# Kernel tuning notes

Measured on AMD Instinct MI355X. Metric: run time of the kernel, lower is better.

The kernel has to match this reference:

```python
import jax, jax.numpy as jnp
import numpy as np

B, NQ, NKV, D, H = 2, 2048, 2048, 2048, 16
HD = D // H


def setup_inputs() -> dict:
    key = jax.random.key(0)
    ks = jax.random.split(key, 9)
    return {
        "x": jax.random.normal(ks[0], (B, NQ, D), jnp.float32),
        "k": jax.random.normal(ks[1], (B, H, NKV, HD), jnp.float32),
        "v": jax.random.normal(ks[2], (B, H, NKV, HD), jnp.float32),
        "tier_labels": jax.random.randint(ks[3], (B, NKV), 0, 3),
        "padding_mask": jnp.zeros((B, NKV), dtype=bool),
        "q_w": jax.random.normal(ks[4], (D, D), jnp.float32) * (D ** -0.5),
        "q_b": jax.random.normal(ks[5], (D,), jnp.float32) * 0.02,
        "out_w": jax.random.normal(ks[6], (D, D), jnp.float32) * (D ** -0.5),
        "out_b": jax.random.normal(ks[7], (D,), jnp.float32) * 0.02,
        "tier_bias": jax.random.normal(ks[8], (3,), jnp.float32) * 0.1,
    }


def reference(x, k, v, tier_labels, padding_mask, q_w, q_b, out_w, out_b, tier_bias):
    b, n_q, d = x.shape
    h, n_kv, hd = k.shape[1], k.shape[2], k.shape[3]
    scale = hd ** -0.5
    # q projection: torch Linear is x @ W.T + b
    q = x @ q_w.T + q_b                         # [b, n_q, d]
    q = q.reshape(b, n_q, h, hd).transpose(0, 2, 1, 3)  # [b, h, n_q, hd]
    attn = jnp.einsum("bhqd,bhkd->bhqk", q, k) * scale  # [b, h, n_q, n_kv]
    # additive tier bias gathered per kv token
    attn = attn + tier_bias[tier_labels][:, None, None, :]
    # causal mask: triu(-inf, diagonal=n_kv - n_q + 1)
    causal = jnp.triu(jnp.full((n_q, n_kv), -jnp.inf, dtype=x.dtype), k=n_kv - n_q + 1)
    attn = attn + causal
    # padding mask -> -inf
    attn = jnp.where(padding_mask[:, None, None, :], -jnp.inf, attn)
    attn = jax.nn.softmax(attn, axis=-1)
    out = jnp.einsum("bhqk,bhkd->bhqd", attn, v)  # [b, h, n_q, hd]
    out = out.transpose(0, 2, 1, 3).reshape(b, n_q, d)
    return out @ out_w.T + out_b
```

## Files before the change

### kernel.cpp

```cpp
#include <hip/hip_runtime.h>
#include <stdint.h>

typedef unsigned short u16;
typedef __attribute__((ext_vector_type(8))) short short8;
typedef __attribute__((ext_vector_type(4))) float f32x4;

#define B_   2
#define NQ_  2048
#define NKV_ 2048
#define D_   2048
#define H_   16
#define HD_  128
#define MM_  (B_*NQ_)

__device__ __forceinline__ u16 f2bf(float f) {
  uint32_t u = __float_as_uint(f);
  u += 0x7fffu + ((u >> 16) & 1u);
  return (u16)(u >> 16);
}

__device__ __forceinline__ void gload_lds16(const void* g, void* l) {
  __builtin_amdgcn_global_load_lds(
      (const __attribute__((address_space(1))) void*)g,
      (__attribute__((address_space(3))) void*)l, 16, 0, 0);
}

__global__ __launch_bounds__(256) void cast_bf16(const float* __restrict__ src,
                                                 u16* __restrict__ dst, int n8) {
  int i = blockIdx.x * 256 + threadIdx.x;
  if (i >= n8) return;
  const float4* s = (const float4*)src + (size_t)i * 2;
  float4 a = s[0], b = s[1];
  short8 o;
  o[0] = (short)f2bf(a.x); o[1] = (short)f2bf(a.y);
  o[2] = (short)f2bf(a.z); o[3] = (short)f2bf(a.w);
  o[4] = (short)f2bf(b.x); o[5] = (short)f2bf(b.y);
  o[6] = (short)f2bf(b.z); o[7] = (short)f2bf(b.w);
  *((short8*)dst + i) = o;
}

__global__ __launch_bounds__(256) void build_bias(const int* __restrict__ labels,
                                                  const unsigned char* __restrict__ mask,
                                                  const float* __restrict__ tb,
                                                  float* __restrict__ out, int n) {
  int i = blockIdx.x * 256 + threadIdx.x;
  if (i < n) out[i] = mask[i] ? -1e30f : tb[labels[i]];
}

template<int OUT_BF16>
__global__ __launch_bounds__(256, 2) void gemm_bt(
    const u16* __restrict__ A, const u16* __restrict__ W,
    const float* __restrict__ bias, void* __restrict__ Cout,
    int M, int N, int K)
{
  __shared__ u16 As[128 * 64];
  __shared__ u16 Bs[128 * 64];
  const int tid = threadIdx.x;
  const int w = tid >> 6, l = tid & 63;
  const int lr = l & 15, lg = l >> 4;
  const int nbn = N >> 7;
  const int nwg = gridDim.x;
  int bid = blockIdx.x;
  int swz = (bid & 7) * (nwg >> 3) + (bid >> 3);
  const int bm = swz / nbn, bn = swz % nbn;
  const int wm = w >> 1, wn = w & 1;

  f32x4 acc[4][4] = {};

  const int sr = w * 32 + (l >> 3);
  const int sc = l & 7;

  for (int kt = 0; kt < K; kt += 64) {
#pragma unroll
    for (int i = 0; i < 4; ++i) {
      int r = sr + i * 8;
      int gc = kt + ((sc ^ (r & 7)) << 3);
      gload_lds16(A + (size_t)(bm * 128 + r) * K + gc, (char*)As + (w * 32 + i * 8) * 128);
      gload_lds16(W + (size_t)(bn * 128 + r) * K + gc, (char*)Bs + (w * 32 + i * 8) * 128);
    }
    __syncthreads();
#pragma unroll
    for (int ks = 0; ks < 2; ++ks) {
      short8 av[4], bv[4];
#pragma unroll
      for (int mf = 0; mf < 4; ++mf) {
        int row = wm * 64 + mf * 16 + lr;
        int pch = (ks * 4 + lg) ^ (row & 7);
        av[mf] = *(const short8*)((const char*)As + row * 128 + pch * 16);
      }
#pragma unroll
      for (int nf = 0; nf < 4; ++nf) {
        int row = wn * 64 + nf * 16 + lr;
        int pch = (ks * 4 + lg) ^ (row & 7);
        bv[nf] = *(const short8*)((const char*)Bs + row * 128 + pch * 16);
      }
#pragma unroll
      for (int mf = 0; mf < 4; ++mf)
#pragma unroll
        for (int nf = 0; nf < 4; ++nf)
          acc[mf][nf] = __builtin_amdgcn_mfma_f32_16x16x32_bf16(av[mf], bv[nf], acc[mf][nf], 0, 0, 0);
    }
    __syncthreads();
  }

  const int row0 = bm * 128 + wm * 64;
  const int col0 = bn * 128 + wn * 64;
#pragma unroll
  for (int nf = 0; nf < 4; ++nf) {
    int col = col0 + nf * 16 + lr;
    float bb = bias[col];
#pragma unroll
    for (int mf = 0; mf < 4; ++mf) {
#pragma unroll
      for (int r = 0; r < 4; ++r) {
        size_t row = (size_t)(row0 + mf * 16 + lg * 4 + r);
        float vv = acc[mf][nf][r] + bb;
        if (OUT_BF16) ((u16*)Cout)[row * N + col] = f2bf(vv);
        else          ((float*)Cout)[row * N + col] = vv;
      }
    }
  }
}

__global__ __launch_bounds__(256, 2) void attn_fwd(
    const u16* __restrict__ Q, const u16* __restrict__ Kg,
    const u16* __restrict__ Vg, const float* __restrict__ biaskv,
    u16* __restrict__ AO)
{
  __shared__ u16 Ks[64 * 128];
  __shared__ u16 Vt[128 * 72];
  __shared__ u16 Ps[4][16 * 72];

  const int tid = threadIdx.x;
  const int w = tid >> 6, l = tid & 63;
  const int lr = l & 15, lg = l >> 4;

  int bid = blockIdx.x;
  int swz = (bid & 7) * 128 + (bid >> 3);
  const int qt = 31 - (swz & 31);
  const int h  = (swz >> 5) & 15;
  const int b  = swz >> 9;

  const size_t kvbase = ((size_t)(b * H_ + h)) * NKV_ * HD_;
  const u16* Kh = Kg + kvbase;
  const u16* Vh = Vg + kvbase;
  const float* bkv = biaskv + b * NKV_;

  const int q0 = qt * 64 + w * 16;
  short8 aq[4];
  {
    const u16* qp = Q + (size_t)(b * NQ_ + q0 + lr) * D_ + h * HD_ + lg * 8;
#pragma unroll
    for (int ks = 0; ks < 4; ++ks) aq[ks] = *(const short8*)(qp + ks * 32);
  }

  f32x4 o[8] = {};
  float m[4], ln[4];
#pragma unroll
  for (int r = 0; r < 4; ++r) { m[r] = -1e30f; ln[r] = 0.f; }

  const int ntile = qt + 1;
  for (int kvt = 0; kvt < ntile; ++kvt) {
    const int kv0 = kvt * 64;
#pragma unroll
    for (int i = 0; i < 4; ++i) {
      int r = w * 16 + i * 4 + lg;
      int c = lr ^ (r & 7);
      gload_lds16(Kh + (size_t)(kv0 + r) * HD_ + c * 8, (char*)Ks + (w * 16 + i * 4) * 256);
    }
    {
      const u16* vp = Vh + (size_t)(kv0 + l) * HD_ + w * 32;
#pragma unroll
      for (int j = 0; j < 4; ++j) {
        short8 vv = *(const short8*)(vp + j * 8);
#pragma unroll
        for (int e = 0; e < 8; ++e)
          Vt[(w * 32 + j * 8 + e) * 72 + l] = (u16)vv[e];
      }
    }
    __syncthreads();

    f32x4 s[4];
#pragma unroll
    for (int nf = 0; nf < 4; ++nf) {
      f32x4 c = {};
#pragma unroll
      for (int ks = 0; ks < 4; ++ks) {
        int row = nf * 16 + lr;
        int pch = (ks * 4 + lg) ^ (row & 7);
        short8 bv = *(const short8*)((const char*)Ks + row * 256 + pch * 16);
        c = __builtin_amdgcn_mfma_f32_16x16x32_bf16(aq[ks], bv, c, 0, 0, 0);
      }
      s[nf] = c;
    }

    float sv[4][4];
#pragma unroll
    for (int nf = 0; nf < 4; ++nf) {
      int kv = kv0 + nf * 16 + lr;
      float bb = bkv[kv];
#pragma unroll
      for (int r = 0; r < 4; ++r) {
        float v = s[nf][r] * 0.08838834764831845f + bb;
        if (kvt == ntile - 1) {
          int q = q0 + lg * 4 + r;
          if (kv > q) v = -1e30f;
        }
        sv[nf][r] = v;
      }
    }

    float pm[4];
#pragma unroll
    for (int r = 0; r < 4; ++r)
      pm[r] = fmaxf(fmaxf(sv[0][r], sv[1][r]), fmaxf(sv[2][r], sv[3][r]));
#pragma unroll
    for (int off = 1; off < 16; off <<= 1)
#pragma unroll
      for (int r = 0; r < 4; ++r)
        pm[r] = fmaxf(pm[r], __shfl_xor(pm[r], off, 64));

    float alpha[4], mn[4], ps[4];
#pragma unroll
    for (int r = 0; r < 4; ++r) {
      mn[r] = fmaxf(m[r], pm[r]);
      alpha[r] = __expf(m[r] - mn[r]);
      m[r] = mn[r];
      ps[r] = 0.f;
    }

    u16* Pw = &Ps[w][0];
#pragma unroll
    for (int nf = 0; nf < 4; ++nf)
#pragma unroll
      for (int r = 0; r < 4; ++r) {
        float p = __expf(sv[nf][r] - mn[r]);
        ps[r] += p;
        Pw[(lg * 4 + r) * 72 + nf * 16 + lr] = f2bf(p);
      }

#pragma unroll
    for (int off = 1; off < 16; off <<= 1)
#pragma unroll
      for (int r = 0; r < 4; ++r)
        ps[r] += __shfl_xor(ps[r], off, 64);

#pragma unroll
    for (int r = 0; r < 4; ++r) ln[r] = ln[r] * alpha[r] + ps[r];

#pragma unroll
    for (int cf = 0; cf < 8; ++cf)
#pragma unroll
      for (int r = 0; r < 4; ++r)
        o[cf][r] *= alpha[r];

#pragma unroll
    for (int ks = 0; ks < 2; ++ks) {
      short8 ap = *(const short8*)((const char*)Pw + lr * 144 + ks * 64 + lg * 16);
#pragma unroll
      for (int nf = 0; nf < 8; ++nf) {
        short8 bv = *(const short8*)((const char*)Vt + (nf * 16 + lr) * 144 + ks * 64 + lg * 16);
        o[nf] = __builtin_amdgcn_mfma_f32_16x16x32_bf16(ap, bv, o[nf], 0, 0, 0);
      }
    }
    __syncthreads();
  }

#pragma unroll
  for (int r = 0; r < 4; ++r) {
    float inv = ln[r] > 0.f ? 1.f / ln[r] : 0.f;
    size_t row = (size_t)(b * NQ_ + q0 + lg * 4 + r);
#pragma unroll
    for (int nf = 0; nf < 8; ++nf)
      AO[row * D_ + h * HD_ + nf * 16 + lr] = f2bf(o[nf][r] * inv);
  }
}

extern "C" void kernel_launch(void* const* d_in, const int* in_sizes, int n_in,
                              void* d_out, int out_size, void* d_ws, size_t ws_size,
                              hipStream_t stream) {
  const float* x     = (const float*)d_in[0];
  const float* k     = (const float*)d_in[1];
  const float* v     = (const float*)d_in[2];
  const int*   labels = (const int*)d_in[3];
  const unsigned char* mask = (const unsigned char*)d_in[4];
  const float* q_w   = (const float*)d_in[5];
  const float* q_b   = (const float*)d_in[6];
  const float* out_w = (const float*)d_in[7];
  const float* out_b = (const float*)d_in[8];
  const float* tbias = (const float*)d_in[9];

  char* ws = (char*)d_ws;
  u16* x_bf  = (u16*)(ws + 0);
  u16* qw_bf = (u16*)(ws + 16777216);
  u16* ow_bf = (u16*)(ws + 25165824);
  u16* k_bf  = (u16*)(ws + 33554432);
  u16* v_bf  = (u16*)(ws + 50331648);
  u16* q_bf  = (u16*)(ws + 67108864);
  u16* ao_bf = (u16*)(ws + 83886080);
  float* bkv = (float*)(ws + 100663296);

  cast_bf16<<<4096, 256, 0, stream>>>(x,     x_bf,  1048576);
  cast_bf16<<<2048, 256, 0, stream>>>(q_w,   qw_bf,  524288);
  cast_bf16<<<2048, 256, 0, stream>>>(out_w, ow_bf,  524288);
  cast_bf16<<<4096, 256, 0, stream>>>(k,     k_bf,  1048576);
  cast_bf16<<<4096, 256, 0, stream>>>(v,     v_bf,  1048576);
  build_bias<<<16, 256, 0, stream>>>(labels, mask, tbias, bkv, B_ * NKV_);

  gemm_bt<1><<<512, 256, 0, stream>>>(x_bf, qw_bf, q_b, (void*)q_bf, MM_, D_, D_);
  attn_fwd<<<1024, 256, 0, stream>>>(q_bf, k_bf, v_bf, bkv, ao_bf);
  gemm_bt<0><<<512, 256, 0, stream>>>(ao_bf, ow_bf, out_b, d_out, MM_, D_, D_);
}
```

Before: 404.0 us.

## Pair causal q-tiles per block, double-buffer K/V, compute softmax in registers with exp2

Each attention block now handles two query tiles (qt and 31-qt) that share K/V loads, which balances causal work across blocks and halves the grid. The K/V tiles are double-buffered so global loads for the next tile overlap compute on the current one. The softmax scale and log2e are folded into the Q projection epilogue and the bias, so the kernel can use exp2. QK^T is computed transposed so P stays in registers and is permuted with lane shuffles instead of going through LDS. MFMA sections get raised wave priority via s_setprio. The cost is higher register pressure from two accumulator sets and extra shuffle traffic.

```diff
diff --git a/kernel.cpp b/kernel.cpp
--- a/kernel.cpp
+++ b/kernel.cpp
@@ -4,6 +4,7 @@
 typedef unsigned short u16;
 typedef __attribute__((ext_vector_type(8))) short short8;
 typedef __attribute__((ext_vector_type(4))) float f32x4;
+typedef __attribute__((ext_vector_type(4))) uint32_t u32x4;
 
 #define B_   2
 #define NQ_  2048
@@ -12,6 +13,8 @@
 #define H_   16
 #define HD_  128
 #define MM_  (B_*NQ_)
+#define LOG2E 1.4426950408889634f
+#define QSCALE (0.08838834764831845f * 1.4426950408889634f)
 
 __device__ __forceinline__ u16 f2bf(float f) {
   uint32_t u = __float_as_uint(f);
@@ -44,14 +47,14 @@
                                                   const float* __restrict__ tb,
                                                   float* __restrict__ out, int n) {
   int i = blockIdx.x * 256 + threadIdx.x;
-  if (i < n) out[i] = mask[i] ? -1e30f : tb[labels[i]];
+  if (i < n) out[i] = mask[i] ? -1e30f : tb[labels[i]] * LOG2E;
 }
 
 template<int OUT_BF16>
 __global__ __launch_bounds__(256, 2) void gemm_bt(
     const u16* __restrict__ A, const u16* __restrict__ W,
     const float* __restrict__ bias, void* __restrict__ Cout,
-    int M, int N, int K)
+    int M, int N, int K, float escale)
 {
   __shared__ u16 As[128 * 64];
   __shared__ u16 Bs[128 * 64];
@@ -114,12 +117,119 @@
 #pragma unroll
       for (int r = 0; r < 4; ++r) {
         size_t row = (size_t)(row0 + mf * 16 + lg * 4 + r);
-        float vv = acc[mf][nf][r] + bb;
+        float vv = (acc[mf][nf][r] + bb) * escale;
         if (OUT_BF16) ((u16*)Cout)[row * N + col] = f2bf(vv);
         else          ((float*)Cout)[row * N + col] = vv;
       }
     }
   }
+}
+
+__device__ __forceinline__ void softmax16(
+    const f32x4 s[4], const f32x4 bias4[4], bool diag, int qrow, int kv0,
+    int lr, int lg, float& m, float& d, f32x4 o[8], short8 ap[2])
+{
+  float sv[4][4];
+  float pm = -3e38f;
+#pragma unroll
+  for (int nf = 0; nf < 4; ++nf)
+#pragma unroll
+    for (int r = 0; r < 4; ++r) {
+      float v = s[nf][r] + bias4[nf][r];
+      if (diag) {
+        int kv = kv0 + nf * 16 + lg * 4 + r;
+        if (kv > qrow) v = -1e30f;
+      }
+      sv[nf][r] = v;
+      pm = fmaxf(pm, v);
+    }
+  pm = fmaxf(pm, __shfl_xor(pm, 16));
+  pm = fmaxf(pm, __shfl_xor(pm, 32));
+  float mn = fmaxf(m, pm);
+  float al = __builtin_exp2f(m - mn);
+  m = mn;
+  float ps = 0.f;
+  uint32_t pk0[4], pk1[4];
+#pragma unroll
+  for (int nf = 0; nf < 4; ++nf) {
+    float p0 = __builtin_exp2f(sv[nf][0] - mn);
+    float p1 = __builtin_exp2f(sv[nf][1] - mn);
+    float p2 = __builtin_exp2f(sv[nf][2] - mn);
+    float p3 = __builtin_exp2f(sv[nf][3] - mn);
+    ps += (p0 + p1) + (p2 + p3);
+    pk0[nf] = (uint32_t)f2bf(p0) | ((uint32_t)f2bf(p1) << 16);
+    pk1[nf] = (uint32_t)f2bf(p2) | ((uint32_t)f2bf(p3) << 16);
+  }
+  ps += __shfl_xor(ps, 16);
+  ps += __shfl_xor(ps, 32);
+  d = d * al + ps;
+  float alr[4];
+#pragma unroll
+  for (int r = 0; r < 4; ++r) alr[r] = __shfl(al, lg * 4 + r);
+#pragma unroll
+  for (int nf = 0; nf < 8; ++nf) {
+    o[nf][0] *= alr[0]; o[nf][1] *= alr[1];
+    o[nf][2] *= alr[2]; o[nf][3] *= alr[3];
+  }
+#pragma unroll
+  for (int ks = 0; ks < 2; ++ks) {
+    uint32_t rr[4];
+#pragma unroll
+    for (int i = 0; i < 4; ++i) {
+      uint32_t c0 = ((lg & 1) == (i >> 1)) ? pk0[2 * ks] : pk0[2 * ks + 1];
+      uint32_t c1 = ((lg & 1) == (i >> 1)) ? pk1[2 * ks] : pk1[2 * ks + 1];
+      uint32_t contrib = (i & 1) ? c1 : c0;
+      int srclg = (lg & 1) * 2 + ((i >> 1) ^ (lg >> 1));
+      rr[i] = (uint32_t)__shfl((int)contrib, lr + 16 * srclg);
+    }
+    u32x4 t4;
+    t4[0] = (lg & 2) ? rr[2] : rr[0];
+    t4[1] = (lg & 2) ? rr[3] : rr[1];
+    t4[2] = (lg & 2) ? rr[0] : rr[2];
+    t4[3] = (lg & 2) ? rr[1] : rr[3];
+    ap[ks] = __builtin_bit_cast(short8, t4);
+  }
+}
+
+template<int WA>
+__device__ __forceinline__ void compute_tile(
+    const u16* __restrict__ ksb, const u16* __restrict__ vtb,
+    const short8 aqB[4], const short8 aqA[4],
+    f32x4 oB[8], f32x4 oA[8],
+    float& mB, float& dB, float& mA, float& dA,
+    const f32x4 bias4[4], bool diagB, bool diagA,
+    int qrowB, int qrowA, int kv0, int lr, int lg)
+{
+  f32x4 sB[4] = {}, sA[4] = {};
+  __builtin_amdgcn_s_setprio(1);
+#pragma unroll
+  for (int nf = 0; nf < 4; ++nf) {
+#pragma unroll
+    for (int ks = 0; ks < 4; ++ks) {
+      int row = nf * 16 + lr;
+      int pch = (ks * 4 + lg) ^ (row & 7);
+      short8 bk = *(const short8*)((const char*)ksb + row * 256 + pch * 16);
+      sB[nf] = __builtin_amdgcn_mfma_f32_16x16x32_bf16(bk, aqB[ks], sB[nf], 0, 0, 0);
+      if (WA) sA[nf] = __builtin_amdgcn_mfma_f32_16x16x32_bf16(bk, aqA[ks], sA[nf], 0, 0, 0);
+    }
+  }
+  __builtin_amdgcn_s_setprio(0);
+
+  short8 apB[2], apA[2];
+  softmax16(sB, bias4, diagB, qrowB, kv0, lr, lg, mB, dB, oB, apB);
+  if (WA) softmax16(sA, bias4, diagA, qrowA, kv0, lr, lg, mA, dA, oA, apA);
+
+  __builtin_amdgcn_s_setprio(1);
+#pragma unroll
+  for (int ks = 0; ks < 2; ++ks) {
+#pragma unroll
+    for (int nf = 0; nf < 8; ++nf) {
+      short8 bv = *(const short8*)((const char*)vtb + (nf * 16 + lr) * 144 + ks * 64 + lg * 16);
+      oB[nf] = __builtin_amdgcn_mfma_f32_16x16x32_bf16(apB[ks], bv, oB[nf], 0, 0, 0);
+      if (WA) oA[nf] = __builtin_amdgcn_mfma_f32_16x16x32_bf16(apA[ks], bv, oA[nf], 0, 0, 0);
+    }
+  }
+  __builtin_amdgcn_s_setprio(0);
 }
 
 __global__ __launch_bounds__(256, 2) void attn_fwd(
@@ -127,152 +237,121 @@
     const u16* __restrict__ Vg, const float* __restrict__ biaskv,
     u16* __restrict__ AO)
 {
-  __shared__ u16 Ks[64 * 128];
-  __shared__ u16 Vt[128 * 72];
-  __shared__ u16 Ps[4][16 * 72];
+  __shared__ u16 Ks[2][64 * 128];
+  __shared__ u16 Vt[2][128 * 72];
 
   const int tid = threadIdx.x;
   const int w = tid >> 6, l = tid & 63;
   const int lr = l & 15, lg = l >> 4;
 
-  int bid = blockIdx.x;
-  int swz = (bid & 7) * 128 + (bid >> 3);
-  const int qt = 31 - (swz & 31);
-  const int h  = (swz >> 5) & 15;
-  const int b  = swz >> 9;
-
-  const size_t kvbase = ((size_t)(b * H_ + h)) * NKV_ * HD_;
+  const int bid = blockIdx.x;
+  const int bh = bid & 31, pi = bid >> 5;
+  const int b = bh >> 4, h = bh & 15;
+  const int qtA = pi, qtB = 31 - pi;
+
+  const size_t kvbase = ((size_t)bh) * NKV_ * HD_;
   const u16* Kh = Kg + kvbase;
   const u16* Vh = Vg + kvbase;
   const float* bkv = biaskv + b * NKV_;
 
-  const int q0 = qt * 64 + w * 16;
-  short8 aq[4];
+  const int q0A = qtA * 64 + w * 16;
+  const int q0B = qtB * 64 + w * 16;
+
+  short8 aqA[4], aqB[4];
   {
-    const u16* qp = Q + (size_t)(b * NQ_ + q0 + lr) * D_ + h * HD_ + lg * 8;
-#pragma unroll
-    for (int ks = 0; ks < 4; ++ks) aq[ks] = *(const short8*)(qp + ks * 32);
-  }
-
-  f32x4 o[8] = {};
-  float m[4], ln[4];
-#pragma unroll
-  for (int r = 0; r < 4; ++r) { m[r] = -1e30f; ln[r] = 0.f; }
-
-  const int ntile = qt + 1;
-  for (int kvt = 0; kvt < ntile; ++kvt) {
-    const int kv0 = kvt * 64;
+    const u16* qpA = Q + (size_t)(b * NQ_ + q0A + lr) * D_ + h * HD_ + lg * 8;
+    const u16* qpB = Q + (size_t)(b * NQ_ + q0B + lr) * D_ + h * HD_ + lg * 8;
+#pragma unroll
+    for (int ks = 0; ks < 4; ++ks) {
+      aqA[ks] = *(const short8*)(qpA + ks * 32);
+      aqB[ks] = *(const short8*)(qpB + ks * 32);
+    }
+  }
+
+  f32x4 oA[8] = {}, oB[8] = {};
+  float mA = -1e30f, mB = -1e30f, dA = 0.f, dB = 0.f;
+
+  short8 vv[4];
+  {
 #pragma unroll
     for (int i = 0; i < 4; ++i) {
       int r = w * 16 + i * 4 + lg;
       int c = lr ^ (r & 7);
-      gload_lds16(Kh + (size_t)(kv0 + r) * HD_ + c * 8, (char*)Ks + (w * 16 + i * 4) * 256);
-    }
-    {
-      const u16* vp = Vh + (size_t)(kv0 + l) * HD_ + w * 32;
-#pragma unroll
-      for (int j = 0; j < 4; ++j) {
-        short8 vv = *(const short8*)(vp + j * 8);
+      gload_lds16(Kh + (size_t)r * HD_ + c * 8, (char*)&Ks[0][0] + (w * 16 + i * 4) * 256);
+    }
+    const u16* vp = Vh + (size_t)l * HD_ + w * 32;
+#pragma unroll
+    for (int j = 0; j < 4; ++j) vv[j] = *(const short8*)(vp + j * 8);
+#pragma unroll
+    for (int j = 0; j < 4; ++j)
+#pragma unroll
+      for (int e = 0; e < 8; ++e)
+        Vt[0][(w * 32 + j * 8 + e) * 72 + l] = (u16)vv[j][e];
+  }
+  __syncthreads();
+
+  int cur = 0;
+  for (int kvt = 0; kvt <= qtB; ++kvt) {
+    const int kv0 = kvt * 64;
+    const bool haveNext = (kvt < qtB);
+    if (haveNext) {
+      const int kvn = kv0 + 64;
+#pragma unroll
+      for (int i = 0; i < 4; ++i) {
+        int r = w * 16 + i * 4 + lg;
+        int c = lr ^ (r & 7);
+        gload_lds16(Kh + (size_t)(kvn + r) * HD_ + c * 8,
+                    (char*)&Ks[cur ^ 1][0] + (w * 16 + i * 4) * 256);
+      }
+      const u16* vp = Vh + (size_t)(kvn + l) * HD_ + w * 32;
+#pragma unroll
+      for (int j = 0; j < 4; ++j) vv[j] = *(const short8*)(vp + j * 8);
+    }
+
+    f32x4 bias4[4];
+#pragma unroll
+    for (int nf = 0; nf < 4; ++nf)
+      bias4[nf] = *(const f32x4*)(bkv + kv0 + nf * 16 + lg * 4);
+
+    if (kvt <= qtA)
+      compute_tile<1>(&Ks[cur][0], &Vt[cur][0], aqB, aqA, oB, oA, mB, dB, mA, dA,
+                      bias4, kvt == qtB, kvt == qtA, q0B + lr, q0A + lr, kv0, lr, lg);
+    else
+      compute_tile<0>(&Ks[cur][0], &Vt[cur][0], aqB, aqA, oB, oA, mB, dB, mA, dA,
+                      bias4, kvt == qtB, false, q0B + lr, q0A + lr, kv0, lr, lg);
+
+    if (haveNext) {
+#pragma unroll
+      for (int j = 0; j < 4; ++j)
 #pragma unroll
         for (int e = 0; e < 8; ++e)
-          Vt[(w * 32 + j * 8 + e) * 72 + l] = (u16)vv[e];
-      }
+          Vt[cur ^ 1][(w * 32 + j * 8 + e) * 72 + l] = (u16)vv[j][e];
     }
     __syncthreads();
-
-    f32x4 s[4];
-#pragma unroll
-    for (int nf = 0; nf < 4; ++nf) {
-      f32x4 c = {};
-#pragma unroll
-      for (int ks = 0; ks < 4; ++ks) {
-        int row = nf * 16 + lr;
-        int pch = (ks * 4 + lg) ^ (row & 7);
-        short8 bv = *(const short8*)((const char*)Ks + row * 256 + pch * 16);
-        c = __builtin_amdgcn_mfma_f32_16x16x32_bf16(aq[ks], bv, c, 0, 0, 0);
-      }
-      s[nf] = c;
-    }
-
-    float sv[4][4];
-#pragma unroll
-    for (int nf = 0; nf < 4; ++nf) {
-      int kv = kv0 + nf * 16 + lr;
-      float bb = bkv[kv];
-#pragma unroll
-      for (int r = 0; r < 4; ++r) {
-        float v = s[nf][r] * 0.08838834764831845f + bb;
-        if (kvt == ntile - 1) {
-          int q = q0 + lg * 4 + r;
-          if (kv > q) v = -1e30f;
-        }
-        sv[nf][r] = v;
-      }
-    }
-
-    float pm[4];
-#pragma unroll
-    for (int r = 0; r < 4; ++r)
-      pm[r] = fmaxf(fmaxf(sv[0][r], sv[1][r]), fmaxf(sv[2][r], sv[3][r]));
-#pragma unroll
-    for (int off = 1; off < 16; off <<= 1)
-#pragma unroll
-      for (int r = 0; r < 4; ++r)
-        pm[r] = fmaxf(pm[r], __shfl_xor(pm[r], off, 64));
-
-    float alpha[4], mn[4], ps[4];
-#pragma unroll
-    for (int r = 0; r < 4; ++r) {
-      mn[r] = fmaxf(m[r], pm[r]);
-      alpha[r] = __expf(m[r] - mn[r]);
-      m[r] = mn[r];
-      ps[r] = 0.f;
-    }
-
-    u16* Pw = &Ps[w][0];
-#pragma unroll
-    for (int nf = 0; nf < 4; ++nf)
-#pragma unroll
-      for (int r = 0; r < 4; ++r) {
-        float p = __expf(sv[nf][r] - mn[r]);
-        ps[r] += p;
-        Pw[(lg * 4 + r) * 72 + nf * 16 + lr] = f2bf(p);
-      }
-
-#pragma unroll
-    for (int off = 1; off < 16; off <<= 1)
-#pragma unroll
-      for (int r = 0; r < 4; ++r)
-        ps[r] += __shfl_xor(ps[r], off, 64);
-
-#pragma unroll
-    for (int r = 0; r < 4; ++r) ln[r] = ln[r] * alpha[r] + ps[r];
-
-#pragma unroll
-    for (int cf = 0; cf < 8; ++cf)
-#pragma unroll
-      for (int r = 0; r < 4; ++r)
-        o[cf][r] *= alpha[r];
-
-#pragma unroll
-    for (int ks = 0; ks < 2; ++ks) {
-      short8 ap = *(const short8*)((const char*)Pw + lr * 144 + ks * 64 + lg * 16);
-#pragma unroll
-      for (int nf = 0; nf < 8; ++nf) {
-        short8 bv = *(const short8*)((const char*)Vt + (nf * 16 + lr) * 144 + ks * 64 + lg * 16);
-        o[nf] = __builtin_amdgcn_mfma_f32_16x16x32_bf16(ap, bv, o[nf], 0, 0, 0);
-      }
-    }
-    __syncthreads();
-  }
-
+    cur ^= 1;
+  }
+
+  float dvB[4], dvA[4];
 #pragma unroll
   for (int r = 0; r < 4; ++r) {
-    float inv = ln[r] > 0.f ? 1.f / ln[r] : 0.f;
-    size_t row = (size_t)(b * NQ_ + q0 + lg * 4 + r);
+    dvB[r] = __shfl(dB, lg * 4 + r);
+    dvA[r] = __shfl(dA, lg * 4 + r);
+  }
+#pragma unroll
+  for (int r = 0; r < 4; ++r) {
+    float inv = 1.f / dvB[r];
+    size_t row = (size_t)(b * NQ_ + q0B + lg * 4 + r);
 #pragma unroll
     for (int nf = 0; nf < 8; ++nf)
-      AO[row * D_ + h * HD_ + nf * 16 + lr] = f2bf(o[nf][r] * inv);
+      AO[row * D_ + h * HD_ + nf * 16 + lr] = f2bf(oB[nf][r] * inv);
+  }
+#pragma unroll
+  for (int r = 0; r < 4; ++r) {
+    float inv = 1.f / dvA[r];
+    size_t row = (size_t)(b * NQ_ + q0A + lg * 4 + r);
+#pragma unroll
+    for (int nf = 0; nf < 8; ++nf)
+      AO[row * D_ + h * HD_ + nf * 16 + lr] = f2bf(oA[nf][r] * inv);
   }
 }
 
@@ -307,7 +386,7 @@
   cast_bf16<<<4096, 256, 0, stream>>>(v,     v_bf,  1048576);
   build_bias<<<16, 256, 0, stream>>>(labels, mask, tbias, bkv, B_ * NKV_);
 
-  gemm_bt<1><<<512, 256, 0, stream>>>(x_bf, qw_bf, q_b, (void*)q_bf, MM_, D_, D_);
-  attn_fwd<<<1024, 256, 0, stream>>>(q_bf, k_bf, v_bf, bkv, ao_bf);
-  gemm_bt<0><<<512, 256, 0, stream>>>(ao_bf, ow_bf, out_b, d_out, MM_, D_, D_);
-}
+  gemm_bt<1><<<512, 256, 0, stream>>>(x_bf, qw_bf, q_b, (void*)q_bf, MM_, D_, D_, QSCALE);
+  attn_fwd<<<512, 256, 0, stream>>>(q_bf, k_bf, v_bf, bkv, ao_bf);
+  gemm_bt<0><<<512, 256, 0, stream>>>(ao_bf, ow_bf, out_b, d_out, MM_, D_, D_, 1.0f);
+}
```

New measurement: 398.1 us. About the same (-1.5%).
